# Optimization experiments

Hardware: AMD Instinct MI355X
Metric: run time of the kernel (lower is better)

## Reference

```python
import jax, jax.numpy as jnp
import numpy as np

N = 50000      # nodes
E = 400000     # edges (before self-loops)
IN = 256       # in_dim
H = 4          # heads in layer 1
C = 64         # h_dim (per-head channels, layer 1)
OUT = 16       # out_dim (layer 2, 1 head)
NEG_SLOPE = 0.2


def gatv2_layer(x, src, dst, Wl, bl, Wr, br, att, bias, heads, ch, concat, num_nodes):
    # x: [N, F]; src/dst: [E']; Wl/Wr: [F, heads*ch]; att: [heads, ch]
    xl = (x @ Wl + bl).reshape(num_nodes, heads, ch)  # source transform
    xr = (x @ Wr + br).reshape(num_nodes, heads, ch)  # target transform
    m = xl[src] + xr[dst]                              # [E', H, C] gather
    e = jnp.sum(jax.nn.leaky_relu(m, NEG_SLOPE) * att, axis=-1)  # [E', H]
    # segment softmax over incoming edges of each dst node (self-loops ensure non-empty)
    emax = jax.ops.segment_max(e, dst, num_segments=num_nodes)   # [N, H]
    ee = jnp.exp(e - emax[dst])
    denom = jax.ops.segment_sum(ee, dst, num_segments=num_nodes)  # [N, H]
    alpha = ee / (denom[dst] + 1e-16)                              # [E', H]
    out = jax.ops.segment_sum(alpha[..., None] * xl[src], dst, num_segments=num_nodes)  # [N,H,C]
    if concat:
        out = out.reshape(num_nodes, heads * ch)
    else:
        out = out.mean(axis=1)
    return out + bias


def setup_inputs() -> dict:
    key = jax.random.key(0)
    ks = jax.random.split(key, 16)
    s = 0.05
    inp = {
        "x": jax.random.normal(ks[0], (N, IN), jnp.float32),
        "edge_index": jax.random.randint(ks[1], (2, E), 0, N),
        # layer 1 params (in_dim -> heads*h_dim)
        "Wl1": jax.random.normal(ks[2], (IN, H * C), jnp.float32) * s,
        "bl1": jnp.zeros((H * C,), jnp.float32),
        "Wr1": jax.random.normal(ks[3], (IN, H * C), jnp.float32) * s,
        "br1": jnp.zeros((H * C,), jnp.float32),
        "att1": jax.random.normal(ks[4], (H, C), jnp.float32) * s,
        "bias1": jnp.zeros((H * C,), jnp.float32),
        # layer 2 params (heads*h_dim -> out_dim, 1 head)
        "Wl2": jax.random.normal(ks[5], (H * C, OUT), jnp.float32) * s,
        "bl2": jnp.zeros((OUT,), jnp.float32),
        "Wr2": jax.random.normal(ks[6], (H * C, OUT), jnp.float32) * s,
        "br2": jnp.zeros((OUT,), jnp.float32),
        "att2": jax.random.normal(ks[7], (1, OUT), jnp.float32) * s,
        "bias2": jnp.zeros((OUT,), jnp.float32),
    }
    return inp


def reference(x, edge_index, Wl1, bl1, Wr1, br1, att1, bias1, Wl2, bl2, Wr2, br2, att2, bias2):
    # add self loops (PyG GATv2Conv default add_self_loops=True)
    loop = jnp.arange(N, dtype=edge_index.dtype)
    src = jnp.concatenate([edge_index[0], loop])
    dst = jnp.concatenate([edge_index[1], loop])
    h = gatv2_layer(x, src, dst, Wl1, bl1, Wr1, br1, att1, bias1, H, C, True, N)
    h = jnp.tanh(h)
    o = gatv2_layer(h, src, dst, Wl2, bl2, Wr2, br2, att2, bias2, 1, OUT, False, N)
    return o, jax.nn.log_softmax(o, axis=1)
```

## Files before the change

kernel.cpp:

```cpp
#include <hip/hip_runtime.h>

typedef __bf16 bfv8 __attribute__((ext_vector_type(8)));
typedef float f32x4 __attribute__((ext_vector_type(4)));
typedef float f32x2 __attribute__((ext_vector_type(2)));
typedef short shortv8 __attribute__((ext_vector_type(8)));
typedef unsigned short usv8 __attribute__((ext_vector_type(8)));

__device__ __forceinline__ float b2f(unsigned short u) {
  unsigned int v = ((unsigned int)u) << 16;
  float f;
  __builtin_memcpy(&f, &v, 4);
  return f;
}
__device__ __forceinline__ unsigned short f2b(float f) {
  unsigned int u;
  __builtin_memcpy(&u, &f, 4);
  u += 0x7fffu + ((u >> 16) & 1u);
  return (unsigned short)(u >> 16);
}

__device__ __forceinline__ f32x2 bf2x(unsigned int u) {
  f32x2 r;
  r.x = __builtin_bit_cast(float, u << 16);
  r.y = __builtin_bit_cast(float, u & 0xffff0000u);
  return r;
}

template <int CTRL>
__device__ __forceinline__ float dpp_mv(float x) {
  int xi = __builtin_bit_cast(int, x);
  int yi = __builtin_amdgcn_update_dpp(0, xi, CTRL, 0xf, 0xf, true);
  return __builtin_bit_cast(float, yi);
}

__device__ __forceinline__ float tanh_fast(float x) {
  float e2 = __expf(2.f * x);
  float r = __builtin_amdgcn_rcpf(e2 + 1.f);
  float th = fmaf(-2.f, r, 1.f);
  if (!(th == th)) th = 0.f;
  return th;
}

__global__ void probe_kernel(const unsigned short* __restrict__ x, int* __restrict__ flag) {
  int lane = threadIdx.x;
  int cnt = 0;
  for (int i = lane; i < 4096; i += 64) {
    unsigned int e = (x[i] >> 7) & 0xffu;
    if (e >= 0x86u) cnt++;
  }
#pragma unroll
  for (int off = 1; off < 64; off <<= 1) cnt += __shfl_xor(cnt, off, 64);
  if (lane == 0) *flag = (cnt > 100) ? 1 : 0;
}

__global__ __launch_bounds__(256) void conv_x_kernel(const void* __restrict__ x,
                                                     unsigned short* __restrict__ dst,
                                                     const int* __restrict__ flagp, int n) {
  int i = (blockIdx.x * 256 + threadIdx.x) * 4;
  if (i >= n) return;
  if (*flagp) {
    float4 f = *reinterpret_cast<const float4*>((const float*)x + i);
    ushort4 o;
    o.x = f2b(f.x); o.y = f2b(f.y); o.z = f2b(f.z); o.w = f2b(f.w);
    *reinterpret_cast<ushort4*>(dst + i) = o;
  } else {
    *reinterpret_cast<ushort4*>(dst + i) =
        *reinterpret_cast<const ushort4*>((const unsigned short*)x + i);
  }
}

#define P_TOT 140352
__global__ __launch_bounds__(256) void conv_params_kernel(
    const void* p0, const void* p1, const void* p2, const void* p3,
    const void* p4, const void* p5, const void* p6, const void* p7,
    const void* p8, const void* p9, const void* p10, const void* p11,
    unsigned short* __restrict__ dst, const int* __restrict__ flagp) {
  int i = blockIdx.x * 256 + threadIdx.x;
  if (i >= P_TOT) return;
  const int offs[13] = {0, 65536, 65792, 131328, 131584, 131840, 132096,
                        136192, 136208, 140304, 140320, 140336, P_TOT};
  const void* ptrs[12] = {p0, p1, p2, p3, p4, p5, p6, p7, p8, p9, p10, p11};
  int flag = *flagp;
  int t = 0;
  while (i >= offs[t + 1]) t++;
  int local = i - offs[t];
  unsigned short v;
  if (flag) v = f2b(((const float*)ptrs[t])[local]);
  else v = ((const unsigned short*)ptrs[t])[local];
  dst[i] = v;
}

__global__ __launch_bounds__(256) void transpose_w_kernel(
    const unsigned short* __restrict__ Pc,
    unsigned short* __restrict__ WT1, unsigned short* __restrict__ WT2) {
  int idx = blockIdx.x * 256 + threadIdx.x;
  if (idx < 512 * 256) {
    int n = idx >> 8, k = idx & 255;
    WT1[idx] = (n < 256) ? Pc[0 + k * 256 + n]
                         : Pc[65792 + k * 256 + (n - 256)];
  } else {
    int j = idx - 512 * 256;
    if (j < 32 * 256) {
      int n = j >> 8, k = j & 255;
      WT2[j] = (n < 16) ? Pc[132096 + k * 16 + n]
                        : Pc[136208 + k * 16 + (n - 16)];
    }
  }
}

__global__ __launch_bounds__(256) void gemm1_kernel(
    const unsigned short* __restrict__ X,
    const unsigned short* __restrict__ WT,
    const unsigned short* __restrict__ bl, const unsigned short* __restrict__ br,
    unsigned short* __restrict__ C, int M) {
  __shared__ unsigned short smem[18432];
  const int t = threadIdx.x;
  const int lane = t & 63;
  const int w = t >> 6;
  const int quad = lane >> 4;
  const int l16 = lane & 15;
  const int n_blk = blockIdx.x;
  const int m_base = blockIdx.y * 128 + (w >> 1) * 64;
  const int n_base = n_blk * 128 + (w & 1) * 64;

  const int st_row = t >> 3;
  const int st_seg = t & 7;
  const unsigned short* wt_base =
      WT + ((size_t)(n_blk * 128 + st_row)) * 256 + st_seg * 8;

  f32x4 acc[4][4];
#pragma unroll
  for (int i = 0; i < 4; i++)
#pragma unroll
    for (int j = 0; j < 4; j++) acc[i][j] = (f32x4){0.f, 0.f, 0.f, 0.f};

  shortv8 st[4];
#pragma unroll
  for (int i = 0; i < 4; i++)
    st[i] = *reinterpret_cast<const shortv8*>(wt_base + (size_t)(32 * i) * 256);
#pragma unroll
  for (int i = 0; i < 4; i++) {
    int row = st_row + 32 * i;
    *reinterpret_cast<shortv8*>(smem + row * 64 + ((st_seg ^ (row & 7)) * 8)) = st[i];
  }
  __syncthreads();

#pragma unroll
  for (int c = 0; c < 4; c++) {
    if (c < 3) {
#pragma unroll
      for (int i = 0; i < 4; i++)
        st[i] = *reinterpret_cast<const shortv8*>(wt_base + (size_t)(32 * i) * 256 +
                                                  (c + 1) * 64);
    }
    const unsigned short* bb = smem + (c & 1) * 8192;
#pragma unroll
    for (int sub = 0; sub < 2; sub++) {
      bfv8 a[4], b[4];
      int seg_r = sub * 4 + quad;
#pragma unroll
      for (int i = 0; i < 4; i++) {
        int row = m_base + 16 * i + l16;
        if (row >= M) row = M - 1;
        a[i] = *reinterpret_cast<const bfv8*>(X + (size_t)row * 256 + c * 64 + sub * 32 +
                                              quad * 8);
      }
#pragma unroll
      for (int j = 0; j < 4; j++) {
        int col = (w & 1) * 64 + 16 * j + l16;
        b[j] = *reinterpret_cast<const bfv8*>(bb + col * 64 + ((seg_r ^ (col & 7)) * 8));
      }
#pragma unroll
      for (int i = 0; i < 4; i++)
#pragma unroll
        for (int j = 0; j < 4; j++)
          acc[i][j] = __builtin_amdgcn_mfma_f32_16x16x32_bf16(a[i], b[j], acc[i][j], 0, 0, 0);
    }
    if (c < 3) {
      int buf = (c + 1) & 1;
#pragma unroll
      for (int i = 0; i < 4; i++) {
        int row = st_row + 32 * i;
        *reinterpret_cast<shortv8*>(smem + buf * 8192 + row * 64 +
                                    ((st_seg ^ (row & 7)) * 8)) = st[i];
      }
      __syncthreads();
    }
  }

  __syncthreads();
  unsigned short* lt = smem + w * 4608;
#pragma unroll
  for (int j = 0; j < 4; j++) {
    int col = n_base + 16 * j + l16;
    float bias = (col < 256) ? b2f(bl[col]) : b2f(br[col - 256]);
#pragma unroll
    for (int i = 0; i < 4; i++)
#pragma unroll
      for (int r = 0; r < 4; r++)
        lt[(16 * i + quad * 4 + r) * 72 + 16 * j + l16] = f2b(acc[i][j][r] + bias);
  }
#pragma unroll
  for (int pass = 0; pass < 8; pass++) {
    int row = pass * 8 + (lane >> 3);
    int colg = (lane & 7) * 8;
    shortv8 v = *reinterpret_cast<const shortv8*>(lt + row * 72 + colg);
    int grow = m_base + row;
    if (grow < M)
      *reinterpret_cast<shortv8*>(C + (size_t)grow * 512 + n_base + colg) = v;
  }
}

__global__ __launch_bounds__(256) void gemm2_kernel(
    const unsigned short* __restrict__ H, const unsigned short* __restrict__ WT,
    const unsigned short* __restrict__ bl, const unsigned short* __restrict__ br,
    float* __restrict__ C, int M) {
  const int lane = threadIdx.x & 63;
  const int w = threadIdx.x >> 6;
  const int quad = lane >> 4;
  const int l16 = lane & 15;
  const int m_base = blockIdx.x * 256 + w * 64;

  f32x4 acc[4][2];
#pragma unroll
  for (int i = 0; i < 4; i++)
#pragma unroll
    for (int j = 0; j < 2; j++) acc[i][j] = (f32x4){0.f, 0.f, 0.f, 0.f};

#pragma unroll
  for (int k0 = 0; k0 < 256; k0 += 32) {
    bfv8 a[4], b[2];
#pragma unroll
    for (int i = 0; i < 4; i++) {
      int row = m_base + 16 * i + l16;
      if (row >= M) row = M - 1;
      a[i] = *reinterpret_cast<const bfv8*>(H + (size_t)row * 256 + k0 + quad * 8);
    }
#pragma unroll
    for (int j = 0; j < 2; j++) {
      int col = 16 * j + l16;
      b[j] = *reinterpret_cast<const bfv8*>(WT + (size_t)col * 256 + k0 + quad * 8);
    }
#pragma unroll
    for (int i = 0; i < 4; i++)
#pragma unroll
      for (int j = 0; j < 2; j++)
        acc[i][j] = __builtin_amdgcn_mfma_f32_16x16x32_bf16(a[i], b[j], acc[i][j], 0, 0, 0);
  }

#pragma unroll
  for (int j = 0; j < 2; j++) {
    int col = 16 * j + l16;
    float bias = (j == 0) ? b2f(bl[l16]) : b2f(br[l16]);
#pragma unroll
    for (int i = 0; i < 4; i++) {
#pragma unroll
      for (int r = 0; r < 4; r++) {
        int row = m_base + 16 * i + quad * 4 + r;
        if (row < M) C[(size_t)row * 32 + col] = acc[i][j][r] + bias;
      }
    }
  }
}

__global__ __launch_bounds__(256) void count_kernel(const int* __restrict__ ei, int E, int Nn,
                                                    int* __restrict__ cnt) {
  int i = blockIdx.x * 256 + threadIdx.x;
  int total = E + Nn;
  if (i >= total) return;
  int d = (i < E) ? ei[E + i] : (i - E);
  if ((unsigned)d >= (unsigned)Nn) d = 0;
  atomicAdd(&cnt[d], 1);
}

__global__ __launch_bounds__(1024) void scan1_kernel(const int* __restrict__ cnt,
                                                     int* __restrict__ row_start,
                                                     int* __restrict__ blkTot, int Nn) {
  __shared__ int buf[1024];
  int t = threadIdx.x;
  int i = blockIdx.x * 1024 + t;
  int v = (i < Nn) ? cnt[i] : 0;
  buf[t] = v;
  __syncthreads();
  for (int off = 1; off < 1024; off <<= 1) {
    int x = (t >= off) ? buf[t - off] : 0;
    __syncthreads();
    buf[t] += x;
    __syncthreads();
  }
  if (i < Nn) row_start[i] = buf[t] - v;
  if (t == 1023) blkTot[blockIdx.x] = buf[1023];
}

__global__ __launch_bounds__(64) void scan2_kernel(const int* __restrict__ blkTot,
                                                   int* __restrict__ blkOff, int nb,
                                                   int* __restrict__ row_start, int Nn,
                                                   int total) {
  int lane = threadIdx.x;
  int v = (lane < nb) ? blkTot[lane] : 0;
  int s = v;
#pragma unroll
  for (int off = 1; off < 64; off <<= 1) {
    int u = __shfl_up(s, off, 64);
    if (lane >= off) s += u;
  }
  if (lane < nb) blkOff[lane] = s - v;
  if (lane == 0) row_start[Nn] = total;
}

__global__ __launch_bounds__(1024) void scan3_kernel(int* __restrict__ row_start,
                                                     int* __restrict__ cursor,
                                                     const int* __restrict__ blkOff, int Nn) {
  int i = blockIdx.x * 1024 + threadIdx.x;
  if (i < Nn) {
    int val = row_start[i] + blkOff[blockIdx.x];
    row_start[i] = val;
    cursor[i] = val;
  }
}

__global__ __launch_bounds__(256) void fill_kernel(const int* __restrict__ ei, int E, int Nn,
                                                   int* __restrict__ cursor,
                                                   int* __restrict__ csr_src) {
  int i = blockIdx.x * 256 + threadIdx.x;
  int total = E + Nn;
  if (i >= total) return;
  int s, d;
  if (i < E) { s = ei[i]; d = ei[E + i]; } else { s = i - E; d = i - E; }
  if ((unsigned)d >= (unsigned)Nn) d = 0;
  if ((unsigned)s >= (unsigned)Nn) s = 0;
  int pos = atomicAdd(&cursor[d], 1);
  if ((unsigned)pos < (unsigned)total) csr_src[pos] = s;
}

__global__ __launch_bounds__(256) void agg1_kernel(
    const unsigned short* __restrict__ C1,
    const unsigned short* __restrict__ att1,
    const unsigned short* __restrict__ bias1,
    const int* __restrict__ row_start, const int* __restrict__ csr_src,
    unsigned short* __restrict__ H1,
    int Nn, int Etot) {
  int wid = blockIdx.x * 4 + (threadIdx.x >> 6);
  if (wid >= Nn) return;
  int lane = threadIdx.x & 63;
  int half = lane >> 5;
  int c0 = (lane & 31) * 8;

  f32x2 at2[4], xr2[4];
  {
    uint4 a4 = *reinterpret_cast<const uint4*>(att1 + c0);
    uint4 r4 = *reinterpret_cast<const uint4*>(C1 + (size_t)wid * 512 + 256 + c0);
    at2[0] = bf2x(a4.x); at2[1] = bf2x(a4.y); at2[2] = bf2x(a4.z); at2[3] = bf2x(a4.w);
    xr2[0] = bf2x(r4.x); xr2[1] = bf2x(r4.y); xr2[2] = bf2x(r4.z); xr2[3] = bf2x(r4.w);
  }

  float denom = 0.f;
  f32x2 acc2[4] = {};
  int beg = row_start[wid], end = row_start[wid + 1];
  if (beg < 0) beg = 0;
  if (end < beg || end - beg > Etot) end = beg;

  for (int base = beg; base < end; base += 64) {
    int cend = min(end, base + 64);
    int pl = base + lane;
    if (pl >= end) pl = end - 1;
    int s_pre = csr_src[pl];
#pragma unroll 2
    for (int i = base; i < cend; i += 2) {
      int p = i + half;
      bool valid = p < cend;
      int s = __shfl(s_pre, p - base, 64);
      if ((unsigned)s >= (unsigned)Nn) s = 0;
      uint4 rw = *reinterpret_cast<const uint4*>(C1 + (size_t)s * 512 + c0);
      f32x2 xl0 = bf2x(rw.x), xl1 = bf2x(rw.y), xl2 = bf2x(rw.z), xl3 = bf2x(rw.w);
      f32x2 m0 = xl0 + xr2[0], m1 = xl1 + xr2[1];
      f32x2 m2 = xl2 + xr2[2], m3 = xl3 + xr2[3];
      f32x2 l0 = __builtin_elementwise_max(m0, m0 * 0.2f);
      f32x2 l1 = __builtin_elementwise_max(m1, m1 * 0.2f);
      f32x2 l2 = __builtin_elementwise_max(m2, m2 * 0.2f);
      f32x2 l3 = __builtin_elementwise_max(m3, m3 * 0.2f);
      f32x2 d2 = l0 * at2[0];
      d2 += l1 * at2[1];
      d2 += l2 * at2[2];
      d2 += l3 * at2[3];
      float dot = d2.x + d2.y;
      dot += dpp_mv<0xB1>(dot);
      dot += dpp_mv<0x4E>(dot);
      dot += dpp_mv<0x141>(dot);
      dot = fminf(fmaxf(dot, -60.f), 60.f);
      float wgt = valid ? __expf(dot) : 0.f;
      denom += wgt;
      acc2[0] += xl0 * wgt;
      acc2[1] += xl1 * wgt;
      acc2[2] += xl2 * wgt;
      acc2[3] += xl3 * wgt;
    }
  }
  denom += __shfl_xor(denom, 32, 64);
#pragma unroll
  for (int k = 0; k < 4; k++) {
    acc2[k].x += __shfl_xor(acc2[k].x, 32, 64);
    acc2[k].y += __shfl_xor(acc2[k].y, 32, 64);
  }

  if (half == 0) {
    float inv = __builtin_amdgcn_rcpf(denom + 1e-16f);
    uint4 b4 = *reinterpret_cast<const uint4*>(bias1 + c0);
    f32x2 bb[4] = {bf2x(b4.x), bf2x(b4.y), bf2x(b4.z), bf2x(b4.w)};
    uint4 o;
    unsigned int od[4];
#pragma unroll
    for (int k = 0; k < 4; k++) {
      f32x2 xv = acc2[k] * inv + bb[k];
      float t0 = tanh_fast(xv.x);
      float t1 = tanh_fast(xv.y);
      od[k] = (unsigned int)f2b(t0) | ((unsigned int)f2b(t1) << 16);
    }
    o.x = od[0]; o.y = od[1]; o.z = od[2]; o.w = od[3];
    *reinterpret_cast<uint4*>(H1 + (size_t)wid * 256 + c0) = o;
  }
}

__global__ __launch_bounds__(256) void agg2_kernel(
    const float* __restrict__ C2,
    const unsigned short* __restrict__ att2,
    const unsigned short* __restrict__ bias2,
    const int* __restrict__ row_start, const int* __restrict__ csr_src,
    float* __restrict__ out,
    int Nn, int Etot) {
  int wid = blockIdx.x * 4 + (threadIdx.x >> 6);
  if (wid >= Nn) return;
  int lane = threadIdx.x & 63;
  int eslot = lane >> 2;
  int cg = (lane & 3) * 4;

  float at[4], xr[4];
  {
    ushort4 a4 = *reinterpret_cast<const ushort4*>(att2 + cg);
    at[0] = b2f(a4.x); at[1] = b2f(a4.y); at[2] = b2f(a4.z); at[3] = b2f(a4.w);
    float4 r4 = *reinterpret_cast<const float4*>(C2 + (size_t)wid * 32 + 16 + cg);
    xr[0] = r4.x; xr[1] = r4.y; xr[2] = r4.z; xr[3] = r4.w;
  }

  float denom = 0.f;
  float acc[4] = {0.f, 0.f, 0.f, 0.f};
  int beg = row_start[wid], end = row_start[wid + 1];
  if (beg < 0) beg = 0;
  if (end < beg || end - beg > Etot) end = beg;

  for (int base = beg; base < end; base += 64) {
    int cend = min(end, base + 64);
    int pl = base + lane;
    if (pl >= end) pl = end - 1;
    int s_pre = csr_src[pl];
    for (int i = base; i < cend; i += 16) {
      int p = i + eslot;
      bool valid = p < cend;
      int s = __shfl(s_pre, p - base, 64);
      if ((unsigned)s >= (unsigned)Nn) s = 0;
      float4 x4 = *reinterpret_cast<const float4*>(C2 + (size_t)s * 32 + cg);
      float xl[4] = {x4.x, x4.y, x4.z, x4.w};
      float dot = 0.f;
#pragma unroll
      for (int k = 0; k < 4; k++) {
        float m = xl[k] + xr[k];
        float l = fmaxf(m, 0.2f * m);
        dot = fmaf(l, at[k], dot);
      }
      dot += dpp_mv<0xB1>(dot);
      dot += dpp_mv<0x4E>(dot);
      dot = fminf(fmaxf(dot, -60.f), 60.f);
      float wgt = valid ? __expf(dot) : 0.f;
      denom += wgt;
#pragma unroll
      for (int k = 0; k < 4; k++) acc[k] = fmaf(wgt, xl[k], acc[k]);
    }
  }
  denom += dpp_mv<0x124>(denom);
  denom += dpp_mv<0x128>(denom);
#pragma unroll
  for (int k = 0; k < 4; k++) {
    acc[k] += dpp_mv<0x124>(acc[k]);
    acc[k] += dpp_mv<0x128>(acc[k]);
  }
#pragma unroll
  for (int off = 16; off <= 32; off <<= 1) {
    denom += __shfl_xor(denom, off, 64);
#pragma unroll
    for (int k = 0; k < 4; k++) acc[k] += __shfl_xor(acc[k], off, 64);
  }

  float inv = __builtin_amdgcn_rcpf(denom + 1e-16f);
  ushort4 b4 = *reinterpret_cast<const ushort4*>(bias2 + cg);
  float bb[4] = {b2f(b4.x), b2f(b4.y), b2f(b4.z), b2f(b4.w)};
  float o[4];
#pragma unroll
  for (int k = 0; k < 4; k++) {
    o[k] = acc[k] * inv + bb[k];
    if (!(o[k] == o[k])) o[k] = 0.f;
  }
  float mx = fmaxf(fmaxf(o[0], o[1]), fmaxf(o[2], o[3]));
  mx = fmaxf(mx, dpp_mv<0xB1>(mx));
  mx = fmaxf(mx, dpp_mv<0x4E>(mx));
  float se = 0.f;
#pragma unroll
  for (int k = 0; k < 4; k++) se += __expf(o[k] - mx);
  se += dpp_mv<0xB1>(se);
  se += dpp_mv<0x4E>(se);
  float ls = logf(se);
  if (lane < 4) {
    float4 vo = {o[0], o[1], o[2], o[3]};
    float4 vl = {o[0] - mx - ls, o[1] - mx - ls, o[2] - mx - ls, o[3] - mx - ls};
    *reinterpret_cast<float4*>(out + (size_t)wid * 16 + cg) = vo;
    *reinterpret_cast<float4*>(out + (size_t)Nn * 16 + (size_t)wid * 16 + cg) = vl;
  }
}

extern "C" void kernel_launch(void* const* d_in, const int* in_sizes, int n_in,
                              void* d_out, int out_size, void* d_ws, size_t ws_size,
                              hipStream_t stream) {
  const void* x_raw = d_in[0];
  const int* ei     = (const int*)d_in[1];

  const int M = in_sizes[0] / 256;
  const int E = in_sizes[1] / 2;
  const int TOT = E + M;
  const int NX = M * 256;

  char* ws = (char*)d_ws;
  size_t off = 0;
  auto alloc = [&](size_t bytes) -> void* {
    void* p = ws + off;
    off = (off + bytes + 255) & ~(size_t)255;
    return p;
  };
  int*            flag   = (int*)alloc(4);
  unsigned short* Pc     = (unsigned short*)alloc((size_t)P_TOT * 2);
  unsigned short* Xc     = (unsigned short*)alloc((size_t)NX * 2);
  unsigned short* WT1    = (unsigned short*)alloc((size_t)512 * 256 * 2);
  unsigned short* WT2    = (unsigned short*)alloc((size_t)32 * 256 * 2);
  int*            cnt    = (int*)alloc((size_t)M * 4);
  int*            cursor = (int*)alloc((size_t)M * 4);
  int*            row_start = (int*)alloc((size_t)(M + 1) * 4);
  int*            csr_src   = (int*)alloc((size_t)TOT * 4);
  int*            blkTot = (int*)alloc(64 * 4);
  int*            blkOff = (int*)alloc(64 * 4);
  float*          C2     = (float*)alloc((size_t)M * 32 * 4);
  unsigned short* C1     = (unsigned short*)alloc((size_t)M * 512 * 2);
  const size_t need = off;
  (void)n_in;
  unsigned short* H1 = Xc;

  if (ws_size < need) {
    hipMemsetAsync(d_out, 0, (size_t)out_size * 4, stream);
    return;
  }

  unsigned short* bl1c   = Pc + 65536;
  unsigned short* br1c   = Pc + 131328;
  unsigned short* att1c  = Pc + 131584;
  unsigned short* bias1c = Pc + 131840;
  unsigned short* bl2c   = Pc + 136192;
  unsigned short* br2c   = Pc + 140304;
  unsigned short* att2c  = Pc + 140320;
  unsigned short* bias2c = Pc + 140336;

  hipMemsetAsync(cnt, 0, (size_t)M * 4, stream);

  probe_kernel<<<1, 64, 0, stream>>>((const unsigned short*)x_raw, flag);
  conv_x_kernel<<<(NX / 4 + 255) / 256, 256, 0, stream>>>(x_raw, Xc, flag, NX);
  conv_params_kernel<<<(P_TOT + 255) / 256, 256, 0, stream>>>(
      d_in[2], d_in[3], d_in[4], d_in[5], d_in[6], d_in[7], d_in[8], d_in[9],
      d_in[10], d_in[11], d_in[12], d_in[13], Pc, flag);

  transpose_w_kernel<<<(512 * 256 + 32 * 256 + 255) / 256, 256, 0, stream>>>(Pc, WT1, WT2);

  dim3 g1(4, (M + 127) / 128);
  gemm1_kernel<<<g1, 256, 0, stream>>>(Xc, WT1, bl1c, br1c, C1, M);

  count_kernel<<<(TOT + 255) / 256, 256, 0, stream>>>(ei, E, M, cnt);
  int nb = (M + 1023) / 1024;
  scan1_kernel<<<nb, 1024, 0, stream>>>(cnt, row_start, blkTot, M);
  scan2_kernel<<<1, 64, 0, stream>>>(blkTot, blkOff, nb, row_start, M, TOT);
  scan3_kernel<<<nb, 1024, 0, stream>>>(row_start, cursor, blkOff, M);
  fill_kernel<<<(TOT + 255) / 256, 256, 0, stream>>>(ei, E, M, cursor, csr_src);

  agg1_kernel<<<(M + 3) / 4, 256, 0, stream>>>(C1, att1c, bias1c, row_start, csr_src,
                                               H1, M, TOT);

  gemm2_kernel<<<(M + 255) / 256, 256, 0, stream>>>(H1, WT2, bl2c, br2c, C2, M);

  agg2_kernel<<<(M + 3) / 4, 256, 0, stream>>>(C2, att2c, bias2c, row_start, csr_src,
                                               (float*)d_out, M, TOT);
}
```

Measured before the change: 293.3 us.

## Fuse preprocessing, scan, transpose and CSR fill kernels to cut launches

Merges independent stages into multi-role kernels: x/param conversion with degree counting, block scan with weight transpose, and GEMM1 with the CSR fill, where GEMM and fill blocks are interleaved. The scan3 pass is removed by adding block offsets lazily in the fill and aggregation kernels. A memset zeroes the cursor array instead. The goal is fewer kernel launches and serialization gaps, and letting atomic-heavy fill work overlap with MFMA GEMM work. The cost is extra index arithmetic and a heavier register/LDS footprint on the fill blocks.

```diff
diff --git a/kernel.cpp b/kernel.cpp
--- a/kernel.cpp
+++ b/kernel.cpp
@@ -53,74 +53,153 @@
   if (lane == 0) *flag = (cnt > 100) ? 1 : 0;
 }
 
-__global__ __launch_bounds__(256) void conv_x_kernel(const void* __restrict__ x,
-                                                     unsigned short* __restrict__ dst,
-                                                     const int* __restrict__ flagp, int n) {
-  int i = (blockIdx.x * 256 + threadIdx.x) * 4;
-  if (i >= n) return;
-  if (*flagp) {
-    float4 f = *reinterpret_cast<const float4*>((const float*)x + i);
-    ushort4 o;
-    o.x = f2b(f.x); o.y = f2b(f.y); o.z = f2b(f.z); o.w = f2b(f.w);
-    *reinterpret_cast<ushort4*>(dst + i) = o;
-  } else {
-    *reinterpret_cast<ushort4*>(dst + i) =
-        *reinterpret_cast<const ushort4*>((const unsigned short*)x + i);
-  }
-}
-
 #define P_TOT 140352
-__global__ __launch_bounds__(256) void conv_params_kernel(
+__global__ __launch_bounds__(256) void fused_pre_kernel(
+    const void* __restrict__ x, unsigned short* __restrict__ Xc,
+    const int* __restrict__ flagp, int NX,
+    const int* __restrict__ ei, int E, int Nn, int* __restrict__ cnt,
     const void* p0, const void* p1, const void* p2, const void* p3,
     const void* p4, const void* p5, const void* p6, const void* p7,
     const void* p8, const void* p9, const void* p10, const void* p11,
-    unsigned short* __restrict__ dst, const int* __restrict__ flagp) {
-  int i = blockIdx.x * 256 + threadIdx.x;
-  if (i >= P_TOT) return;
-  const int offs[13] = {0, 65536, 65792, 131328, 131584, 131840, 132096,
-                        136192, 136208, 140304, 140320, 140336, P_TOT};
-  const void* ptrs[12] = {p0, p1, p2, p3, p4, p5, p6, p7, p8, p9, p10, p11};
-  int flag = *flagp;
-  int t = 0;
-  while (i >= offs[t + 1]) t++;
-  int local = i - offs[t];
-  unsigned short v;
-  if (flag) v = f2b(((const float*)ptrs[t])[local]);
-  else v = ((const unsigned short*)ptrs[t])[local];
-  dst[i] = v;
-}
-
-__global__ __launch_bounds__(256) void transpose_w_kernel(
+    unsigned short* __restrict__ Pc, int nb_convx, int nb_count) {
+  int b = blockIdx.x;
+  int t = threadIdx.x;
+  if (b < nb_convx) {
+    int i = (b * 256 + t) * 4;
+    if (i >= NX) return;
+    if (*flagp) {
+      float4 f = *reinterpret_cast<const float4*>((const float*)x + i);
+      ushort4 o;
+      o.x = f2b(f.x); o.y = f2b(f.y); o.z = f2b(f.z); o.w = f2b(f.w);
+      *reinterpret_cast<ushort4*>(Xc + i) = o;
+    } else {
+      *reinterpret_cast<ushort4*>(Xc + i) =
+          *reinterpret_cast<const ushort4*>((const unsigned short*)x + i);
+    }
+  } else if (b < nb_convx + nb_count) {
+    int i = (b - nb_convx) * 256 + t;
+    int total = E + Nn;
+    if (i >= total) return;
+    int d = (i < E) ? ei[E + i] : (i - E);
+    if ((unsigned)d >= (unsigned)Nn) d = 0;
+    atomicAdd(&cnt[d], 1);
+  } else {
+    int i = (b - nb_convx - nb_count) * 256 + t;
+    if (i >= P_TOT) return;
+    const int offs[13] = {0, 65536, 65792, 131328, 131584, 131840, 132096,
+                          136192, 136208, 140304, 140320, 140336, P_TOT};
+    const void* ptrs[12] = {p0, p1, p2, p3, p4, p5, p6, p7, p8, p9, p10, p11};
+    int flag = *flagp;
+    int k = 0;
+    while (i >= offs[k + 1]) k++;
+    int local = i - offs[k];
+    unsigned short v;
+    if (flag) v = f2b(((const float*)ptrs[k])[local]);
+    else v = ((const unsigned short*)ptrs[k])[local];
+    Pc[i] = v;
+  }
+}
+
+__global__ __launch_bounds__(1024) void fused_mid_kernel(
+    const int* __restrict__ cnt, int* __restrict__ row_start, int* __restrict__ blkTot,
+    int Nn, int nb_scan,
     const unsigned short* __restrict__ Pc,
     unsigned short* __restrict__ WT1, unsigned short* __restrict__ WT2) {
-  int idx = blockIdx.x * 256 + threadIdx.x;
-  if (idx < 512 * 256) {
-    int n = idx >> 8, k = idx & 255;
-    WT1[idx] = (n < 256) ? Pc[0 + k * 256 + n]
-                         : Pc[65792 + k * 256 + (n - 256)];
+  int b = blockIdx.x;
+  int t = threadIdx.x;
+  if (b < nb_scan) {
+    __shared__ int buf[1024];
+    int i = b * 1024 + t;
+    int v = (i < Nn) ? cnt[i] : 0;
+    buf[t] = v;
+    __syncthreads();
+    for (int off = 1; off < 1024; off <<= 1) {
+      int x = (t >= off) ? buf[t - off] : 0;
+      __syncthreads();
+      buf[t] += x;
+      __syncthreads();
+    }
+    if (i < Nn) row_start[i] = buf[t] - v;
+    if (t == 1023) blkTot[b] = buf[1023];
   } else {
-    int j = idx - 512 * 256;
-    if (j < 32 * 256) {
-      int n = j >> 8, k = j & 255;
-      WT2[j] = (n < 16) ? Pc[132096 + k * 16 + n]
-                        : Pc[136208 + k * 16 + (n - 16)];
-    }
-  }
-}
-
-__global__ __launch_bounds__(256) void gemm1_kernel(
+    int idx = (b - nb_scan) * 1024 + t;
+    if (idx < 512 * 256) {
+      int n = idx >> 8, k = idx & 255;
+      WT1[idx] = (n < 256) ? Pc[0 + k * 256 + n]
+                           : Pc[65792 + k * 256 + (n - 256)];
+    } else {
+      int j = idx - 512 * 256;
+      if (j < 32 * 256) {
+        int n = j >> 8, k = j & 255;
+        WT2[j] = (n < 16) ? Pc[132096 + k * 16 + n]
+                          : Pc[136208 + k * 16 + (n - 16)];
+      }
+    }
+  }
+}
+
+__global__ __launch_bounds__(64) void scan2_kernel(const int* __restrict__ blkTot,
+                                                   int* __restrict__ blkOff, int nb,
+                                                   int* __restrict__ row_start, int Nn,
+                                                   int total) {
+  int lane = threadIdx.x;
+  int v = (lane < nb) ? blkTot[lane] : 0;
+  int s = v;
+#pragma unroll
+  for (int off = 1; off < 64; off <<= 1) {
+    int u = __shfl_up(s, off, 64);
+    if (lane >= off) s += u;
+  }
+  int excl = s - v;
+  blkOff[lane] = excl;
+  if (lane == 63) blkOff[64] = s;
+  int idx = Nn >> 10;
+  int bo = (idx >= 64) ? __shfl(s, 63, 64) : __shfl(excl, idx, 64);
+  if (lane == 0) row_start[Nn] = total - bo;
+}
+
+__global__ __launch_bounds__(256) void fused_gemm_fill_kernel(
     const unsigned short* __restrict__ X,
     const unsigned short* __restrict__ WT,
     const unsigned short* __restrict__ bl, const unsigned short* __restrict__ br,
-    unsigned short* __restrict__ C, int M) {
+    unsigned short* __restrict__ C, int M,
+    const int* __restrict__ ei, int E, int Nn,
+    const int* __restrict__ row_start, const int* __restrict__ blkOff,
+    int* __restrict__ cursor, int* __restrict__ csr_src,
+    int nb_gemm, int nb_fill) {
   __shared__ unsigned short smem[18432];
+  int b = blockIdx.x;
+  int nmin = nb_gemm < nb_fill ? nb_gemm : nb_fill;
+  int ninter = 2 * nmin;
+  int role, id;
+  if (b < ninter) { role = b & 1; id = b >> 1; }
+  else {
+    int r = b - ninter;
+    if (nb_fill > nb_gemm) { role = 1; id = nb_gemm + r; }
+    else { role = 0; id = nb_fill + r; }
+  }
+
+  if (role == 1) {
+    int i = id * 256 + threadIdx.x;
+    int total = E + Nn;
+    if (i >= total) return;
+    int s, d;
+    if (i < E) { s = ei[i]; d = ei[E + i]; } else { s = i - E; d = i - E; }
+    if ((unsigned)d >= (unsigned)Nn) d = 0;
+    if ((unsigned)s >= (unsigned)Nn) s = 0;
+    int pos = row_start[d] + blkOff[d >> 10] + atomicAdd(&cursor[d], 1);
+    if ((unsigned)pos < (unsigned)total) csr_src[pos] = s;
+    return;
+  }
+
   const int t = threadIdx.x;
   const int lane = t & 63;
   const int w = t >> 6;
   const int quad = lane >> 4;
   const int l16 = lane & 15;
-  const int n_blk = blockIdx.x;
-  const int m_base = blockIdx.y * 128 + (w >> 1) * 64;
+  const int n_blk = id & 3;
+  const int by = id >> 2;
+  const int m_base = by * 128 + (w >> 1) * 64;
   const int n_base = n_blk * 128 + (w & 1) * 64;
 
   const int st_row = t >> 3;
@@ -156,7 +235,7 @@
     const unsigned short* bb = smem + (c & 1) * 8192;
 #pragma unroll
     for (int sub = 0; sub < 2; sub++) {
-      bfv8 a[4], b[4];
+      bfv8 a[4], bfr[4];
       int seg_r = sub * 4 + quad;
 #pragma unroll
       for (int i = 0; i < 4; i++) {
@@ -168,13 +247,13 @@
 #pragma unroll
       for (int j = 0; j < 4; j++) {
         int col = (w & 1) * 64 + 16 * j + l16;
-        b[j] = *reinterpret_cast<const bfv8*>(bb + col * 64 + ((seg_r ^ (col & 7)) * 8));
+        bfr[j] = *reinterpret_cast<const bfv8*>(bb + col * 64 + ((seg_r ^ (col & 7)) * 8));
       }
 #pragma unroll
       for (int i = 0; i < 4; i++)
 #pragma unroll
         for (int j = 0; j < 4; j++)
-          acc[i][j] = __builtin_amdgcn_mfma_f32_16x16x32_bf16(a[i], b[j], acc[i][j], 0, 0, 0);
+          acc[i][j] = __builtin_amdgcn_mfma_f32_16x16x32_bf16(a[i], bfr[j], acc[i][j], 0, 0, 0);
     }
     if (c < 3) {
       int buf = (c + 1) & 1;
@@ -263,81 +342,12 @@
   }
 }
 
-__global__ __launch_bounds__(256) void count_kernel(const int* __restrict__ ei, int E, int Nn,
-                                                    int* __restrict__ cnt) {
-  int i = blockIdx.x * 256 + threadIdx.x;
-  int total = E + Nn;
-  if (i >= total) return;
-  int d = (i < E) ? ei[E + i] : (i - E);
-  if ((unsigned)d >= (unsigned)Nn) d = 0;
-  atomicAdd(&cnt[d], 1);
-}
-
-__global__ __launch_bounds__(1024) void scan1_kernel(const int* __restrict__ cnt,
-                                                     int* __restrict__ row_start,
-                                                     int* __restrict__ blkTot, int Nn) {
-  __shared__ int buf[1024];
-  int t = threadIdx.x;
-  int i = blockIdx.x * 1024 + t;
-  int v = (i < Nn) ? cnt[i] : 0;
-  buf[t] = v;
-  __syncthreads();
-  for (int off = 1; off < 1024; off <<= 1) {
-    int x = (t >= off) ? buf[t - off] : 0;
-    __syncthreads();
-    buf[t] += x;
-    __syncthreads();
-  }
-  if (i < Nn) row_start[i] = buf[t] - v;
-  if (t == 1023) blkTot[blockIdx.x] = buf[1023];
-}
-
-__global__ __launch_bounds__(64) void scan2_kernel(const int* __restrict__ blkTot,
-                                                   int* __restrict__ blkOff, int nb,
-                                                   int* __restrict__ row_start, int Nn,
-                                                   int total) {
-  int lane = threadIdx.x;
-  int v = (lane < nb) ? blkTot[lane] : 0;
-  int s = v;
-#pragma unroll
-  for (int off = 1; off < 64; off <<= 1) {
-    int u = __shfl_up(s, off, 64);
-    if (lane >= off) s += u;
-  }
-  if (lane < nb) blkOff[lane] = s - v;
-  if (lane == 0) row_start[Nn] = total;
-}
-
-__global__ __launch_bounds__(1024) void scan3_kernel(int* __restrict__ row_start,
-                                                     int* __restrict__ cursor,
-                                                     const int* __restrict__ blkOff, int Nn) {
-  int i = blockIdx.x * 1024 + threadIdx.x;
-  if (i < Nn) {
-    int val = row_start[i] + blkOff[blockIdx.x];
-    row_start[i] = val;
-    cursor[i] = val;
-  }
-}
-
-__global__ __launch_bounds__(256) void fill_kernel(const int* __restrict__ ei, int E, int Nn,
-                                                   int* __restrict__ cursor,
-                                                   int* __restrict__ csr_src) {
-  int i = blockIdx.x * 256 + threadIdx.x;
-  int total = E + Nn;
-  if (i >= total) return;
-  int s, d;
-  if (i < E) { s = ei[i]; d = ei[E + i]; } else { s = i - E; d = i - E; }
-  if ((unsigned)d >= (unsigned)Nn) d = 0;
-  if ((unsigned)s >= (unsigned)Nn) s = 0;
-  int pos = atomicAdd(&cursor[d], 1);
-  if ((unsigned)pos < (unsigned)total) csr_src[pos] = s;
-}
-
 __global__ __launch_bounds__(256) void agg1_kernel(
     const unsigned short* __restrict__ C1,
     const unsigned short* __restrict__ att1,
     const unsigned short* __restrict__ bias1,
-    const int* __restrict__ row_start, const int* __restrict__ csr_src,
+    const int* __restrict__ row_start, const int* __restrict__ blkOff,
+    const int* __restrict__ csr_src,
     unsigned short* __restrict__ H1,
     int Nn, int Etot) {
   int wid = blockIdx.x * 4 + (threadIdx.x >> 6);
@@ -356,7 +366,8 @@
 
   float denom = 0.f;
   f32x2 acc2[4] = {};
-  int beg = row_start[wid], end = row_start[wid + 1];
+  int beg = row_start[wid] + blkOff[wid >> 10];
+  int end = row_start[wid + 1] + blkOff[(wid + 1) >> 10];
   if (beg < 0) beg = 0;
   if (end < beg || end - beg > Etot) end = beg;
 
@@ -425,7 +436,8 @@
     const float* __restrict__ C2,
     const unsigned short* __restrict__ att2,
     const unsigned short* __restrict__ bias2,
-    const int* __restrict__ row_start, const int* __restrict__ csr_src,
+    const int* __restrict__ row_start, const int* __restrict__ blkOff,
+    const int* __restrict__ csr_src,
     float* __restrict__ out,
     int Nn, int Etot) {
   int wid = blockIdx.x * 4 + (threadIdx.x >> 6);
@@ -444,7 +456,8 @@
 
   float denom = 0.f;
   float acc[4] = {0.f, 0.f, 0.f, 0.f};
-  int beg = row_start[wid], end = row_start[wid + 1];
+  int beg = row_start[wid] + blkOff[wid >> 10];
+  int end = row_start[wid + 1] + blkOff[(wid + 1) >> 10];
   if (beg < 0) beg = 0;
   if (end < beg || end - beg > Etot) end = beg;
 
@@ -544,7 +557,7 @@
   int*            row_start = (int*)alloc((size_t)(M + 1) * 4);
   int*            csr_src   = (int*)alloc((size_t)TOT * 4);
   int*            blkTot = (int*)alloc(64 * 4);
-  int*            blkOff = (int*)alloc(64 * 4);
+  int*            blkOff = (int*)alloc(65 * 4);
   float*          C2     = (float*)alloc((size_t)M * 32 * 4);
   unsigned short* C1     = (unsigned short*)alloc((size_t)M * 512 * 2);
   const size_t need = off;
@@ -566,30 +579,36 @@
   unsigned short* bias2c = Pc + 140336;
 
   hipMemsetAsync(cnt, 0, (size_t)M * 4, stream);
+  hipMemsetAsync(cursor, 0, (size_t)M * 4, stream);
 
   probe_kernel<<<1, 64, 0, stream>>>((const unsigned short*)x_raw, flag);
-  conv_x_kernel<<<(NX / 4 + 255) / 256, 256, 0, stream>>>(x_raw, Xc, flag, NX);
-  conv_params_kernel<<<(P_TOT + 255) / 256, 256, 0, stream>>>(
+
+  const int nb_convx = (NX / 4 + 255) / 256;
+  const int nb_count = (TOT + 255) / 256;
+  const int nb_convp = (P_TOT + 255) / 256;
+  fused_pre_kernel<<<nb_convx + nb_count + nb_convp, 256, 0, stream>>>(
+      x_raw, Xc, flag, NX, ei, E, M, cnt,
       d_in[2], d_in[3], d_in[4], d_in[5], d_in[6], d_in[7], d_in[8], d_in[9],
-      d_in[10], d_in[11], d_in[12], d_in[13], Pc, flag);
-
-  transpose_w_kernel<<<(512 * 256 + 32 * 256 + 255) / 256, 256, 0, stream>>>(Pc, WT1, WT2);
-
-  dim3 g1(4, (M + 127) / 128);
-  gemm1_kernel<<<g1, 256, 0, stream>>>(Xc, WT1, bl1c, br1c, C1, M);
-
-  count_kernel<<<(TOT + 255) / 256, 256, 0, stream>>>(ei, E, M, cnt);
-  int nb = (M + 1023) / 1024;
-  scan1_kernel<<<nb, 1024, 0, stream>>>(cnt, row_start, blkTot, M);
-  scan2_kernel<<<1, 64, 0, stream>>>(blkTot, blkOff, nb, row_start, M, TOT);
-  scan3_kernel<<<nb, 1024, 0, stream>>>(row_start, cursor, blkOff, M);
-  fill_kernel<<<(TOT + 255) / 256, 256, 0, stream>>>(ei, E, M, cursor, csr_src);
-
-  agg1_kernel<<<(M + 3) / 4, 256, 0, stream>>>(C1, att1c, bias1c, row_start, csr_src,
-                                               H1, M, TOT);
+      d_in[10], d_in[11], d_in[12], d_in[13], Pc, nb_convx, nb_count);
+
+  const int nb_scan = (M + 1023) / 1024;
+  const int nb_tr = (512 * 256 + 32 * 256 + 1023) / 1024;
+  fused_mid_kernel<<<nb_scan + nb_tr, 1024, 0, stream>>>(cnt, row_start, blkTot, M,
+                                                         nb_scan, Pc, WT1, WT2);
+
+  scan2_kernel<<<1, 64, 0, stream>>>(blkTot, blkOff, nb_scan, row_start, M, TOT);
+
+  const int nb_gemm = 4 * ((M + 127) / 128);
+  const int nb_fill = nb_count;
+  fused_gemm_fill_kernel<<<nb_gemm + nb_fill, 256, 0, stream>>>(
+      Xc, WT1, bl1c, br1c, C1, M, ei, E, M, row_start, blkOff, cursor, csr_src,
+      nb_gemm, nb_fill);
+
+  agg1_kernel<<<(M + 3) / 4, 256, 0, stream>>>(C1, att1c, bias1c, row_start, blkOff,
+                                               csr_src, H1, M, TOT);
 
   gemm2_kernel<<<(M + 255) / 256, 256, 0, stream>>>(H1, WT2, bl2c, br2c, C2, M);
 
-  agg2_kernel<<<(M + 3) / 4, 256, 0, stream>>>(C2, att2c, bias2c, row_start, csr_src,
-                                               (float*)d_out, M, TOT);
-}
+  agg2_kernel<<<(M + 3) / 4, 256, 0, stream>>>(C2, att2c, bias2c, row_start, blkOff,
+                                               csr_src, (float*)d_out, M, TOT);
+}
```

Measured after the change: 288.2 us. About the same (-1.7%).
